# Kernel optimization log

Measured on AMD Instinct MI355X. Metric: run time of the kernel, lower is better.

The kernel has to match this reference:

```python
import jax, jax.numpy as jnp
import numpy as np

EPS = 1e-8
SIM_THRESHOLD = 0.5


def _conv(x, src, dst, W, b):
    # Gather per-edge endpoint features: x_j = source, x_i = target (PyG default flow)
    x_j = x[src]
    x_i = x[dst]
    # Cosine similarity per edge
    dot = jnp.sum(x_i * x_j, axis=1)
    denom = jnp.maximum(jnp.linalg.norm(x_i, axis=1) * jnp.linalg.norm(x_j, axis=1), EPS)
    sim = dot / denom
    mask = (sim > SIM_THRESHOLD).astype(x.dtype)[:, None]
    msg = x_j * mask
    # Scatter-add aggregate into target nodes
    agg = jax.ops.segment_sum(msg, dst, num_segments=x.shape[0])
    # update: Linear
    return agg @ W.T + b


def setup_inputs() -> dict:
    key = jax.random.key(0)
    k1, k2, k3, k4, k5 = jax.random.split(key, 5)
    N, E, D_IN, D_HID, D_OUT = 50000, 800000, 128, 256, 64
    x = jax.random.normal(k1, (N, D_IN), dtype=jnp.float32)
    edge_index = jax.random.randint(k2, (2, E), 0, N, dtype=jnp.int64)
    # Xavier-uniform linear weights, zero-ish bias
    lim1 = float(np.sqrt(6.0 / (D_IN + D_HID)))
    lim2 = float(np.sqrt(6.0 / (D_HID + D_OUT)))
    W1 = jax.random.uniform(k3, (D_HID, D_IN), minval=-lim1, maxval=lim1, dtype=jnp.float32)
    b1 = jnp.zeros((D_HID,), dtype=jnp.float32)
    W2 = jax.random.uniform(k4, (D_OUT, D_HID), minval=-lim2, maxval=lim2, dtype=jnp.float32)
    b2 = jnp.zeros((D_OUT,), dtype=jnp.float32)
    return {"x": x, "edge_index": edge_index, "W1": W1, "b1": b1, "W2": W2, "b2": b2}


def reference(x, edge_index, W1, b1, W2, b2):
    N = x.shape[0]
    # add self-loops
    loops = jnp.arange(N, dtype=edge_index.dtype)
    src = jnp.concatenate([edge_index[0], loops])
    dst = jnp.concatenate([edge_index[1], loops])
    h = _conv(x, src, dst, W1, b1)
    h = jax.nn.relu(h)  # dropout is identity in eval mode
    out = _conv(h, src, dst, W2, b2)
    return jax.nn.log_softmax(out, axis=-1)
```

## Files before the change

### kernel.cpp

```cpp
#include <hip/hip_runtime.h>
#include <math.h>

#define EPS 1e-8f
#define NB_SORT 256

#if defined(__has_builtin)
#if __has_builtin(__builtin_amdgcn_sdot4)
#define HAVE_SDOT4 1
#endif
#endif

typedef __attribute__((ext_vector_type(8))) short bf16x8;
typedef __attribute__((ext_vector_type(4))) float f32x4;

__device__ __forceinline__ int sdot4i(int a, int b, int c) {
#ifdef HAVE_SDOT4
  return __builtin_amdgcn_sdot4(a, b, c, false);
#else
  return c + ((int)(signed char)(a)) * ((int)(signed char)(b)) +
         ((int)(signed char)(a >> 8)) * ((int)(signed char)(b >> 8)) +
         ((int)(signed char)(a >> 16)) * ((int)(signed char)(b >> 16)) +
         (a >> 24) * (b >> 24);
#endif
}

__device__ __forceinline__ float wave_reduce_sum(float v) {
#pragma unroll
  for (int off = 32; off > 0; off >>= 1)
    v += __shfl_xor(v, off, 64);
  return v;
}

__device__ __forceinline__ float wave_reduce_max(float v) {
#pragma unroll
  for (int off = 32; off > 0; off >>= 1)
    v = fmaxf(v, __shfl_xor(v, off, 64));
  return v;
}

__device__ __forceinline__ float dot4(float4 a, float4 b) {
  return a.x * b.x + a.y * b.y + a.z * b.z + a.w * b.w;
}

__device__ __forceinline__ int clampq(float q) {
  int i = (int)rintf(q);
  return i < -127 ? -127 : (i > 127 ? 127 : i);
}

__device__ __forceinline__ void split_bf16(float x, unsigned int& hi,
                                           unsigned int& lo) {
  unsigned int u = __float_as_uint(x);
  hi = u >> 16;
  float hf = __uint_as_float(u & 0xFFFF0000u);
  float r = x - hf;
  lo = __float_as_uint(r) >> 16;
}

__global__ __launch_bounds__(256) void hist_coarse(const int* __restrict__ dst,
                                                   int* __restrict__ hist_blk,
                                                   int E, int nbuck) {
  __shared__ int lh[1024];
  int t = threadIdx.x, blk = blockIdx.x;
  for (int i = t; i < nbuck; i += 256) lh[i] = 0;
  __syncthreads();
  int ch = (E + NB_SORT - 1) / NB_SORT;
  int lo = blk * ch, hi = min(E, lo + ch);
  for (int e = lo + t; e < hi; e += 256) atomicAdd(&lh[dst[e] >> 6], 1);
  __syncthreads();
  for (int i = t; i < nbuck; i += 256) hist_blk[i * NB_SORT + blk] = lh[i];
}

__global__ __launch_bounds__(256) void scan_local(int* __restrict__ hist,
                                                  int* __restrict__ bsum,
                                                  int nb) {
  __shared__ int tsum[256];
  int t = threadIdx.x;
  int base = blockIdx.x * 1024 + t * 4;
  int v0 = 0, v1 = 0, v2 = 0, v3 = 0;
  if (base + 3 < nb) {
    int4 q = *(const int4*)&hist[base];
    v0 = q.x; v1 = q.y; v2 = q.z; v3 = q.w;
  } else {
    if (base + 0 < nb) v0 = hist[base + 0];
    if (base + 1 < nb) v1 = hist[base + 1];
    if (base + 2 < nb) v2 = hist[base + 2];
  }
  tsum[t] = v0 + v1 + v2 + v3;
  __syncthreads();
  for (int off = 1; off < 256; off <<= 1) {
    int u = 0;
    if (t >= off) u = tsum[t - off];
    __syncthreads();
    if (t >= off) tsum[t] += u;
    __syncthreads();
  }
  int excl = (t == 0) ? 0 : tsum[t - 1];
  int e0 = excl, e1 = excl + v0, e2 = e1 + v1, e3 = e2 + v2;
  if (base + 3 < nb) {
    *(int4*)&hist[base] = make_int4(e0, e1, e2, e3);
  } else {
    if (base + 0 < nb) hist[base + 0] = e0;
    if (base + 1 < nb) hist[base + 1] = e1;
    if (base + 2 < nb) hist[base + 2] = e2;
  }
  if (t == 255) bsum[blockIdx.x] = tsum[255];
}

__global__ __launch_bounds__(256) void scan_bsum(int* __restrict__ bsum,
                                                 int nblk) {
  __shared__ int sh[256];
  int t = threadIdx.x;
  sh[t] = (t < nblk) ? bsum[t] : 0;
  __syncthreads();
  for (int off = 1; off < 256; off <<= 1) {
    int u = 0;
    if (t >= off) u = sh[t - off];
    __syncthreads();
    if (t >= off) sh[t] += u;
    __syncthreads();
  }
  if (t < nblk) bsum[t] = (t == 0) ? 0 : sh[t - 1];
}

__global__ __launch_bounds__(256) void add_bsum(int* __restrict__ hist,
                                                const int* __restrict__ bsum,
                                                int nb) {
  int i = blockIdx.x * blockDim.x + threadIdx.x;
  if (i < nb) hist[i] += bsum[i >> 10];
}

__global__ __launch_bounds__(256) void scatter_coarse(
    const int* __restrict__ src, const int* __restrict__ dst,
    const int* __restrict__ S, int2* __restrict__ epair, int E, int nbuck) {
  __shared__ int lb[1024];
  int t = threadIdx.x, blk = blockIdx.x;
  for (int i = t; i < nbuck; i += 256) lb[i] = S[i * NB_SORT + blk];
  __syncthreads();
  int ch = (E + NB_SORT - 1) / NB_SORT;
  int lo = blk * ch, hi = min(E, lo + ch);
  for (int e = lo + t; e < hi; e += 256) {
    int d = dst[e];
    int pos = atomicAdd(&lb[d >> 6], 1);
    epair[pos] = make_int2(src[e], d);
  }
}

__global__ __launch_bounds__(256) void fine_sort(
    const int2* __restrict__ epair, const int* __restrict__ S,
    int2* __restrict__ spair, int E, int nbuck) {
  __shared__ int fh[64];
  __shared__ int cur[64];
  int b = blockIdx.x, t = threadIdx.x;
  int bstart = S[b * NB_SORT];
  int bend = (b + 1 < nbuck) ? S[(b + 1) * NB_SORT] : E;
  if (t < 64) fh[t] = 0;
  __syncthreads();
  for (int e = bstart + t; e < bend; e += 256)
    atomicAdd(&fh[epair[e].y & 63], 1);
  __syncthreads();
  if (t < 64) {
    int v = fh[t];
    int incl = v;
#pragma unroll
    for (int off = 1; off < 64; off <<= 1) {
      int u = __shfl_up(incl, off, 64);
      if (t >= off) incl += u;
    }
    cur[t] = incl - v;
  }
  __syncthreads();
  for (int e = bstart + t; e < bend; e += 256) {
    int2 p = epair[e];
    int pos = atomicAdd(&cur[p.y & 63], 1);
    spair[bstart + pos] = p;
  }
}

__global__ __launch_bounds__(256) void prep_x(const float* __restrict__ x,
                                              signed char* __restrict__ qx,
                                              float4* __restrict__ nprop,
                                              float* __restrict__ agg,
                                              int N) {
  int node = (int)((blockIdx.x * blockDim.x + threadIdx.x) >> 6);
  int lane = threadIdx.x & 63;
  if (node >= N) return;
  float2 v = *(const float2*)(x + (size_t)node * 128 + lane * 2);
  float ax = fabsf(v.x), ay = fabsf(v.y);
  float mx = wave_reduce_max(fmaxf(ax, ay));
  float l1 = wave_reduce_sum(ax + ay);
  float ss = wave_reduce_sum(v.x * v.x + v.y * v.y);
  float s = mx * (1.0f / 127.0f);
  float inv = (mx > 0.f) ? 127.0f / mx : 0.f;
  int q0 = clampq(v.x * inv), q1 = clampq(v.y * inv);
  unsigned short w = (unsigned short)((q0 & 0xff) | ((q1 & 0xff) << 8));
  ((unsigned short*)(qx + (size_t)node * 128))[lane] = w;
  float l1q = s * wave_reduce_sum((float)(abs(q0) + abs(q1)));
  bool sp = ss > 0.5f * fmaxf(ss, EPS);
  *(float2*)(agg + (size_t)node * 128 + lane * 2) =
      sp ? v : make_float2(0.f, 0.f);
  if (lane == 0)
    nprop[node] = make_float4(sqrtf(ss), s, fmaxf(l1, l1q), 0.f);
}

__global__ __launch_bounds__(256) void prep_h(const float* __restrict__ h,
                                              signed char* __restrict__ qh,
                                              float4* __restrict__ nprop,
                                              float* __restrict__ agg,
                                              int N) {
  int node = (int)((blockIdx.x * blockDim.x + threadIdx.x) >> 6);
  int lane = threadIdx.x & 63;
  if (node >= N) return;
  float4 v = *(const float4*)(h + (size_t)node * 256 + lane * 4);
  float ax = fabsf(v.x), ay = fabsf(v.y), az = fabsf(v.z), aw = fabsf(v.w);
  float mx = wave_reduce_max(fmaxf(fmaxf(ax, ay), fmaxf(az, aw)));
  float l1 = wave_reduce_sum(ax + ay + az + aw);
  float ss = wave_reduce_sum(dot4(v, v));
  float s = mx * (1.0f / 127.0f);
  float inv = (mx > 0.f) ? 127.0f / mx : 0.f;
  int q0 = clampq(v.x * inv), q1 = clampq(v.y * inv);
  int q2 = clampq(v.z * inv), q3 = clampq(v.w * inv);
  int w = (q0 & 0xff) | ((q1 & 0xff) << 8) | ((q2 & 0xff) << 16) | (q3 << 24);
  ((int*)(qh + (size_t)node * 256))[lane] = w;
  float l1q = s * wave_reduce_sum((float)(abs(q0) + abs(q1) + abs(q2) + abs(q3)));
  bool sp = ss > 0.5f * fmaxf(ss, EPS);
  *(float4*)(agg + (size_t)node * 256 + lane * 4) =
      sp ? v : make_float4(0.f, 0.f, 0.f, 0.f);
  if (lane == 0)
    nprop[node] = make_float4(sqrtf(ss), s, fmaxf(l1, l1q), 0.f);
}

template <int D>
__global__ __launch_bounds__(256) void conv_flat(
    const float* __restrict__ xf, const signed char* __restrict__ qt,
    const float4* __restrict__ nprop, const int2* __restrict__ spair,
    float* __restrict__ agg, int E) {
  constexpr int NG = D / 16;
  constexpr int V = D / 64;
  const int e0 = blockIdx.x * 256 + threadIdx.x;
  const int lane = threadIdx.x & 63;
  const bool valid = e0 < E;
  int2 p = valid ? spair[e0] : make_int2(0, 0);
  const int s = p.x, d = p.y;
  float4 nps = nprop[s];
  float4 npd = nprop[d];
  const signed char* srow = qt + (size_t)s * D;
  const signed char* drow = qt + (size_t)d * D;
  int id = 0;
#pragma unroll
  for (int g = 0; g < NG; ++g) {
    int4 a = *(const int4*)(srow + g * 16);
    int4 bq = *(const int4*)(drow + g * 16);
    id = sdot4i(a.x, bq.x, id);
    id = sdot4i(a.y, bq.y, id);
    id = sdot4i(a.z, bq.z, id);
    id = sdot4i(a.w, bq.w, id);
  }
  float denom = fmaxf(nps.x * npd.x, EPS);
  float thr = 0.5f * denom;
  float approx = (nps.y * npd.y) * (float)id;
  float m = 0.5002f * (nps.y * npd.z + npd.y * nps.z) + 2e-6f * denom + 1e-7f;
  bool maybe = valid && (approx > thr - m);
  unsigned long long mask = __ballot(maybe);
  while (mask) {
    int ln = __ffsll((long long)mask) - 1;
    mask &= mask - 1;
    int es = __shfl(s, ln);
    int ed = __shfl(d, ln);
    float nsx = __shfl(nps.x, ln);
    float ndx = __shfl(npd.x, ln);
    float sv[V], dvv[V];
    if constexpr (V == 2) {
      float2 a = *(const float2*)(xf + (size_t)es * D + lane * 2);
      float2 b = *(const float2*)(xf + (size_t)ed * D + lane * 2);
      sv[0] = a.x; sv[1] = a.y; dvv[0] = b.x; dvv[1] = b.y;
    } else {
      float4 a = *(const float4*)(xf + (size_t)es * D + lane * 4);
      float4 b = *(const float4*)(xf + (size_t)ed * D + lane * 4);
      sv[0] = a.x; sv[1] = a.y; sv[2] = a.z; sv[3] = a.w;
      dvv[0] = b.x; dvv[1] = b.y; dvv[2] = b.z; dvv[3] = b.w;
    }
    float dx = 0.f;
#pragma unroll
    for (int q = 0; q < V; ++q) dx += sv[q] * dvv[q];
    dx = wave_reduce_sum(dx);
    if (dx > 0.5f * fmaxf(nsx * ndx, EPS)) {
      float* arow = agg + (size_t)ed * D + lane * V;
#pragma unroll
      for (int q = 0; q < V; ++q) atomicAdd(&arow[q], sv[q]);
    }
  }
}

__global__ __launch_bounds__(256) void gemm1_mfma(
    const float* __restrict__ A, const float* __restrict__ W,
    const float* __restrict__ bias, float* __restrict__ C, int M) {
  constexpr int K = 128, NN = 256, BM = 128, BK = 32, PK = 40;
  __shared__ unsigned short Ah[BM * PK];
  __shared__ unsigned short Al[BM * PK];
  __shared__ unsigned short Wh[BM * PK];
  __shared__ unsigned short Wl[BM * PK];
  const int tid = threadIdx.x;
  const int m0 = blockIdx.x * BM;
  const int n0 = blockIdx.y * BM;
  const int lane = tid & 63;
  const int wv = tid >> 6;
  const int wr = wv >> 1, wc = wv & 1;
  const int lrow = lane & 15, kg = lane >> 4;
  f32x4 acc[4][4] = {};

  for (int k0 = 0; k0 < K; k0 += BK) {
#pragma unroll
    for (int i = 0; i < 4; ++i) {
      int f = tid + i * 256;
      int r = f >> 3, q = f & 7;
      int gm = m0 + r;
      float4 a = (gm < M) ? *(const float4*)&A[(size_t)gm * K + k0 + q * 4]
                          : make_float4(0.f, 0.f, 0.f, 0.f);
      float4 w = *(const float4*)&W[(size_t)(n0 + r) * K + k0 + q * 4];
      unsigned int h0, h1, h2, h3, l0, l1, l2, l3;
      split_bf16(a.x, h0, l0); split_bf16(a.y, h1, l1);
      split_bf16(a.z, h2, l2); split_bf16(a.w, h3, l3);
      *(uint2*)&Ah[r * PK + q * 4] =
          make_uint2(h0 | (h1 << 16), h2 | (h3 << 16));
      *(uint2*)&Al[r * PK + q * 4] =
          make_uint2(l0 | (l1 << 16), l2 | (l3 << 16));
      split_bf16(w.x, h0, l0); split_bf16(w.y, h1, l1);
      split_bf16(w.z, h2, l2); split_bf16(w.w, h3, l3);
      *(uint2*)&Wh[r * PK + q * 4] =
          make_uint2(h0 | (h1 << 16), h2 | (h3 << 16));
      *(uint2*)&Wl[r * PK + q * 4] =
          make_uint2(l0 | (l1 << 16), l2 | (l3 << 16));
    }
    __syncthreads();
    bf16x8 ah[4], al[4], bh[4], bl[4];
#pragma unroll
    for (int m = 0; m < 4; ++m) {
      int row = wr * 64 + m * 16 + lrow;
      ah[m] = *(const bf16x8*)&Ah[row * PK + kg * 8];
      al[m] = *(const bf16x8*)&Al[row * PK + kg * 8];
    }
#pragma unroll
    for (int n = 0; n < 4; ++n) {
      int row = wc * 64 + n * 16 + lrow;
      bh[n] = *(const bf16x8*)&Wh[row * PK + kg * 8];
      bl[n] = *(const bf16x8*)&Wl[row * PK + kg * 8];
    }
#pragma unroll
    for (int m = 0; m < 4; ++m)
#pragma unroll
      for (int n = 0; n < 4; ++n) {
        acc[m][n] = __builtin_amdgcn_mfma_f32_16x16x32_bf16(ah[m], bh[n],
                                                            acc[m][n], 0, 0, 0);
        acc[m][n] = __builtin_amdgcn_mfma_f32_16x16x32_bf16(ah[m], bl[n],
                                                            acc[m][n], 0, 0, 0);
        acc[m][n] = __builtin_amdgcn_mfma_f32_16x16x32_bf16(al[m], bh[n],
                                                            acc[m][n], 0, 0, 0);
      }
    __syncthreads();
  }

#pragma unroll
  for (int n = 0; n < 4; ++n) {
    int gc = n0 + wc * 64 + n * 16 + lrow;
    float bv = bias[gc];
#pragma unroll
    for (int m = 0; m < 4; ++m) {
      int gr0 = m0 + wr * 64 + m * 16 + kg * 4;
#pragma unroll
      for (int r = 0; r < 4; ++r) {
        int gm = gr0 + r;
        if (gm < M) {
          float v = acc[m][n][r] + bv;
          C[(size_t)gm * NN + gc] = fmaxf(v, 0.f);
        }
      }
    }
  }
}

__global__ __launch_bounds__(256) void split_w2(
    const float* __restrict__ W, unsigned short* __restrict__ Wh,
    unsigned short* __restrict__ Wl, int total4) {
  int i = blockIdx.x * 256 + threadIdx.x;
  if (i >= total4) return;
  float4 w = ((const float4*)W)[i];
  unsigned int h0, h1, h2, h3, l0, l1, l2, l3;
  split_bf16(w.x, h0, l0); split_bf16(w.y, h1, l1);
  split_bf16(w.z, h2, l2); split_bf16(w.w, h3, l3);
  ((uint2*)Wh)[i] = make_uint2(h0 | (h1 << 16), h2 | (h3 << 16));
  ((uint2*)Wl)[i] = make_uint2(l0 | (l1 << 16), l2 | (l3 << 16));
}

__global__ __launch_bounds__(256) void gemm2_mfma_lsm(
    const float* __restrict__ A, const unsigned short* __restrict__ Wh,
    const unsigned short* __restrict__ Wl, const float* __restrict__ bias,
    float* __restrict__ out, int M) {
  constexpr int K = 256;
  const int tid = threadIdx.x;
  const int lane = tid & 63;
  const int wv = tid >> 6;
  const int lrow = lane & 15, kg = lane >> 4;
  const int r0 = blockIdx.x * 128 + wv * 32;
  f32x4 acc[2][4] = {};

  for (int k0 = 0; k0 < K; k0 += 32) {
    bf16x8 ah[2], al[2];
#pragma unroll
    for (int m = 0; m < 2; ++m) {
      int row = r0 + m * 16 + lrow;
      const float* ap = A + (size_t)row * K + k0 + kg * 8;
      float4 a0 = *(const float4*)ap;
      float4 a1 = *(const float4*)(ap + 4);
      unsigned int hh[8], ll[8];
      split_bf16(a0.x, hh[0], ll[0]); split_bf16(a0.y, hh[1], ll[1]);
      split_bf16(a0.z, hh[2], ll[2]); split_bf16(a0.w, hh[3], ll[3]);
      split_bf16(a1.x, hh[4], ll[4]); split_bf16(a1.y, hh[5], ll[5]);
      split_bf16(a1.z, hh[6], ll[6]); split_bf16(a1.w, hh[7], ll[7]);
      bf16x8 th, tl;
#pragma unroll
      for (int j = 0; j < 8; ++j) {
        th[j] = (short)hh[j];
        tl[j] = (short)ll[j];
      }
      ah[m] = th;
      al[m] = tl;
    }
    bf16x8 bh[4], bl[4];
#pragma unroll
    for (int n = 0; n < 4; ++n) {
      int wrow = n * 16 + lrow;
      bh[n] = *(const bf16x8*)&Wh[(size_t)wrow * K + k0 + kg * 8];
      bl[n] = *(const bf16x8*)&Wl[(size_t)wrow * K + k0 + kg * 8];
    }
#pragma unroll
    for (int m = 0; m < 2; ++m)
#pragma unroll
      for (int n = 0; n < 4; ++n) {
        acc[m][n] = __builtin_amdgcn_mfma_f32_16x16x32_bf16(ah[m], bh[n],
                                                            acc[m][n], 0, 0, 0);
        acc[m][n] = __builtin_amdgcn_mfma_f32_16x16x32_bf16(ah[m], bl[n],
                                                            acc[m][n], 0, 0, 0);
        acc[m][n] = __builtin_amdgcn_mfma_f32_16x16x32_bf16(al[m], bh[n],
                                                            acc[m][n], 0, 0, 0);
      }
  }

  float bv[4];
#pragma unroll
  for (int n = 0; n < 4; ++n) bv[n] = bias[n * 16 + lrow];
#pragma unroll
  for (int m = 0; m < 2; ++m)
#pragma unroll
    for (int r = 0; r < 4; ++r) {
      int row = r0 + m * 16 + kg * 4 + r;
      float v[4];
      float mx = -1e30f;
#pragma unroll
      for (int n = 0; n < 4; ++n) {
        v[n] = acc[m][n][r] + bv[n];
        mx = fmaxf(mx, v[n]);
      }
#pragma unroll
      for (int off = 8; off > 0; off >>= 1)
        mx = fmaxf(mx, __shfl_xor(mx, off, 64));
      float s = 0.f;
#pragma unroll
      for (int n = 0; n < 4; ++n) s += expf(v[n] - mx);
#pragma unroll
      for (int off = 8; off > 0; off >>= 1) s += __shfl_xor(s, off, 64);
      float lg = logf(s);
      if (row < M) {
#pragma unroll
        for (int n = 0; n < 4; ++n)
          out[(size_t)row * 64 + n * 16 + lrow] = v[n] - mx - lg;
      }
    }
}

extern "C" void kernel_launch(void* const* d_in, const int* in_sizes, int n_in,
                              void* d_out, int out_size, void* d_ws,
                              size_t ws_size, hipStream_t stream) {
  const float* x  = (const float*)d_in[0];
  const int* eidx = (const int*)d_in[1];
  const float* W1 = (const float*)d_in[2];
  const float* b1 = (const float*)d_in[3];
  const float* W2 = (const float*)d_in[4];
  const float* b2 = (const float*)d_in[5];
  float* out = (float*)d_out;

  const int N = in_sizes[0] / 128;
  const int E = in_sizes[1] / 2;
  const int* src = eidx;
  const int* dst = eidx + E;

  const int nbuck = (N + 63) / 64;
  const int ntot = nbuck * NB_SORT;
  const int nblk2 = (ntot + 1023) / 1024;

  float* agg    = (float*)d_ws;
  float* h      = agg + (size_t)N * 256;
  float4* npx   = (float4*)(h + (size_t)N * 256);
  float4* nph   = npx + N;
  int* S        = (int*)(nph + N);
  int* bsum     = S + ntot;
  int2* spair   = (int2*)(bsum + 256);
  signed char* qh = (signed char*)(spair + E);
  unsigned short* W2h = (unsigned short*)(qh + (size_t)N * 256);
  unsigned short* W2l = W2h + 64 * 256;
  int2* epair   = (int2*)h;
  signed char* qx = (signed char*)(h + (size_t)N * 64);

  split_w2<<<16, 256, 0, stream>>>(W2, W2h, W2l, 64 * 256 / 4);

  hist_coarse<<<NB_SORT, 256, 0, stream>>>(dst, S, E, nbuck);
  scan_local<<<nblk2, 256, 0, stream>>>(S, bsum, ntot);
  scan_bsum<<<1, 256, 0, stream>>>(bsum, nblk2);
  add_bsum<<<(ntot + 255) / 256, 256, 0, stream>>>(S, bsum, ntot);
  scatter_coarse<<<NB_SORT, 256, 0, stream>>>(src, dst, S, epair, E, nbuck);
  fine_sort<<<nbuck, 256, 0, stream>>>(epair, S, spair, E, nbuck);

  const int nblkE = (E + 255) / 256;

  prep_x<<<(N + 3) / 4, 256, 0, stream>>>(x, qx, npx, agg, N);
  conv_flat<128><<<nblkE, 256, 0, stream>>>(x, qx, npx, spair, agg, E);
  gemm1_mfma<<<dim3((N + 127) / 128, 2), 256, 0, stream>>>(agg, W1, b1, h, N);

  prep_h<<<(N + 3) / 4, 256, 0, stream>>>(h, qh, nph, agg, N);
  conv_flat<256><<<nblkE, 256, 0, stream>>>(h, qh, nph, spair, agg, E);
  gemm2_mfma_lsm<<<dim3((N + 127) / 128), 256, 0, stream>>>(agg, W2h, W2l, b2,
                                                            out, N);
}
```

Measured before the change: 296.2 us.

## Split int8 similarity prefilter across lane groups and skip exact check for certain edges

Result: faster. 275.5 us (-7.0%).

```diff
diff --git a/kernel.cpp b/kernel.cpp
--- a/kernel.cpp
+++ b/kernel.cpp
@@ -230,40 +230,65 @@
 }
 
 template <int D>
-__global__ __launch_bounds__(256) void conv_flat(
+__global__ __launch_bounds__(256) void conv_coop(
     const float* __restrict__ xf, const signed char* __restrict__ qt,
     const float4* __restrict__ nprop, const int2* __restrict__ spair,
     float* __restrict__ agg, int E) {
-  constexpr int NG = D / 16;
+  constexpr int G = D / 16;
+  constexpr int EPW = 64 / G;
   constexpr int V = D / 64;
-  const int e0 = blockIdx.x * 256 + threadIdx.x;
-  const int lane = threadIdx.x & 63;
-  const bool valid = e0 < E;
-  int2 p = valid ? spair[e0] : make_int2(0, 0);
+  const int tid = threadIdx.x;
+  const int lane = tid & 63;
+  const int wv = tid >> 6;
+  const int g = lane & (G - 1);
+  const int sub = lane / G;
+  const int e = (blockIdx.x * 4 + wv) * EPW + sub;
+  const bool valid = e < E;
+  int2 p = spair[valid ? e : (E - 1)];
   const int s = p.x, d = p.y;
   float4 nps = nprop[s];
   float4 npd = nprop[d];
-  const signed char* srow = qt + (size_t)s * D;
-  const signed char* drow = qt + (size_t)d * D;
   int id = 0;
-#pragma unroll
-  for (int g = 0; g < NG; ++g) {
-    int4 a = *(const int4*)(srow + g * 16);
-    int4 bq = *(const int4*)(drow + g * 16);
+  {
+    int4 a = *(const int4*)(qt + (size_t)s * D + g * 16);
+    int4 bq = *(const int4*)(qt + (size_t)d * D + g * 16);
     id = sdot4i(a.x, bq.x, id);
     id = sdot4i(a.y, bq.y, id);
     id = sdot4i(a.z, bq.z, id);
     id = sdot4i(a.w, bq.w, id);
   }
+#pragma unroll
+  for (int off = G / 2; off > 0; off >>= 1) id += __shfl_xor(id, off, 64);
   float denom = fmaxf(nps.x * npd.x, EPS);
   float thr = 0.5f * denom;
   float approx = (nps.y * npd.y) * (float)id;
   float m = 0.5002f * (nps.y * npd.z + npd.y * nps.z) + 2e-6f * denom + 1e-7f;
   bool maybe = valid && (approx > thr - m);
-  unsigned long long mask = __ballot(maybe);
-  while (mask) {
-    int ln = __ffsll((long long)mask) - 1;
-    mask &= mask - 1;
+  bool defp = maybe && (approx - m > thr);
+  bool amb = maybe && !defp;
+  unsigned long long defmask = __ballot(defp && g == 0);
+  unsigned long long ambmask = __ballot(amb && g == 0);
+  while (defmask) {
+    int ln = __ffsll((long long)defmask) - 1;
+    defmask &= defmask - 1;
+    int es = __shfl(s, ln);
+    int ed = __shfl(d, ln);
+    float* arow = agg + (size_t)ed * D + lane * V;
+    if constexpr (V == 2) {
+      float2 a = *(const float2*)(xf + (size_t)es * D + lane * 2);
+      atomicAdd(&arow[0], a.x);
+      atomicAdd(&arow[1], a.y);
+    } else {
+      float4 a = *(const float4*)(xf + (size_t)es * D + lane * 4);
+      atomicAdd(&arow[0], a.x);
+      atomicAdd(&arow[1], a.y);
+      atomicAdd(&arow[2], a.z);
+      atomicAdd(&arow[3], a.w);
+    }
+  }
+  while (ambmask) {
+    int ln = __ffsll((long long)ambmask) - 1;
+    ambmask &= ambmask - 1;
     int es = __shfl(s, ln);
     int ed = __shfl(d, ln);
     float nsx = __shfl(nps.x, ln);
@@ -519,14 +544,12 @@
   scatter_coarse<<<NB_SORT, 256, 0, stream>>>(src, dst, S, epair, E, nbuck);
   fine_sort<<<nbuck, 256, 0, stream>>>(epair, S, spair, E, nbuck);
 
-  const int nblkE = (E + 255) / 256;
-
   prep_x<<<(N + 3) / 4, 256, 0, stream>>>(x, qx, npx, agg, N);
-  conv_flat<128><<<nblkE, 256, 0, stream>>>(x, qx, npx, spair, agg, E);
+  conv_coop<128><<<(E + 31) / 32, 256, 0, stream>>>(x, qx, npx, spair, agg, E);
   gemm1_mfma<<<dim3((N + 127) / 128, 2), 256, 0, stream>>>(agg, W1, b1, h, N);
 
   prep_h<<<(N + 3) / 4, 256, 0, stream>>>(h, qh, nph, agg, N);
-  conv_flat<256><<<nblkE, 256, 0, stream>>>(h, qh, nph, spair, agg, E);
+  conv_coop<256><<<(E + 15) / 16, 256, 0, stream>>>(h, qh, nph, spair, agg, E);
   gemm2_mfma_lsm<<<dim3((N + 127) / 128), 256, 0, stream>>>(agg, W2h, W2l, b2,
                                                             out, N);
 }
```
